# Optimization experiments

Hardware: AMD Instinct MI355X
Metric: run time of the kernel (lower is better)

Reference implementation:

```python
import jax, jax.numpy as jnp
import numpy as np

HEADS = 12
EMBED = 768
HEAD_DIM = EMBED // HEADS
SCALING = HEAD_DIM ** (-0.5)


def setup_inputs() -> dict:
    key = jax.random.key(0)
    k1, k2, k3, k4, k5 = jax.random.split(key, 5)
    B, N = 8, 1024
    x = jax.random.normal(k1, (B, N, EMBED), dtype=jnp.float32)
    W_qkv = jax.random.normal(k2, (3 * EMBED, EMBED), dtype=jnp.float32) * 0.02
    b_qkv = jax.random.normal(k3, (3 * EMBED,), dtype=jnp.float32) * 0.02
    W_proj = jax.random.normal(k4, (EMBED, EMBED), dtype=jnp.float32) * 0.02
    b_proj = jax.random.normal(k5, (EMBED,), dtype=jnp.float32) * 0.02
    return {"x": x, "W_qkv": W_qkv, "b_qkv": b_qkv, "W_proj": W_proj, "b_proj": b_proj}


def reference(x, W_qkv, b_qkv, W_proj, b_proj):
    B, N, D = x.shape
    # fused QKV projection: [B, N, 3D]
    qkv = x @ W_qkv.T + b_qkv
    # split last dim as (u=3, h, e) per einops 'b n (u h e) -> u b h n e'
    qkv = qkv.reshape(B, N, 3, HEADS, HEAD_DIM).transpose(2, 0, 3, 1, 4)
    q, k, v = qkv[0], qkv[1], qkv[2]
    # raw dot-product scores (NO pre-softmax scaling, per original)
    sim = jnp.einsum('bhqi,bhki->bhqk', q, k)
    # unusual POST-softmax scaling
    sim = jax.nn.softmax(sim, axis=-1) * SCALING
    att = jnp.einsum('bhnk,bhke->bhne', sim, v)
    att = att.transpose(0, 2, 1, 3).reshape(B, N, D)  # b h n e -> b n (h e)
    return att @ W_proj.T + b_proj
```

## Files before the change

kernel.cpp:

```cpp
#include <hip/hip_runtime.h>

typedef unsigned short u16;
typedef __attribute__((ext_vector_type(8))) short bf16x8;
typedef __attribute__((ext_vector_type(4))) float f32x4;

#define HEADS 12
#define HDIM  64
#define EMBED 768
#define TD    2304
#define SEQ   1024
#define MTOK  8192

__device__ __forceinline__ u16 f2bf(float f) {
  union { float f; unsigned u; } x; x.f = f;
  unsigned r = x.u + 0x7fffu + ((x.u >> 16) & 1u);
  return (u16)(r >> 16);
}

__global__ void cast_kernel(const float* __restrict__ src, u16* __restrict__ dst, int n4) {
  int i = blockIdx.x * blockDim.x + threadIdx.x;
  int st = gridDim.x * blockDim.x;
  for (; i < n4; i += st) {
    float4 v = reinterpret_cast<const float4*>(src)[i];
    ushort4 o;
    o.x = f2bf(v.x); o.y = f2bf(v.y); o.z = f2bf(v.z); o.w = f2bf(v.w);
    reinterpret_cast<ushort4*>(dst)[i] = o;
  }
}

__device__ __forceinline__ void gload_lds16(const u16* g, u16* l) {
  __builtin_amdgcn_global_load_lds(
      (const __attribute__((address_space(1))) unsigned*)g,
      (__attribute__((address_space(3))) unsigned*)l, 16, 0, 0);
}

template <bool OUT_BF16, bool HAS_BIAS>
__global__ __launch_bounds__(256) void gemm_bt(const u16* __restrict__ A,
                                               const u16* __restrict__ B,
                                               const float* __restrict__ bias,
                                               void* __restrict__ Cv, int K) {
  __shared__ u16 As[128 * 32];
  __shared__ u16 Bs[128 * 32];
  const int tid  = threadIdx.x;
  const int wave = tid >> 6, lane = tid & 63;
  const int wr = wave >> 1, wc = wave & 1;
  const int lr = lane & 15, lk = (lane >> 4) * 8;
  const int Ndim = gridDim.y * 128;
  const int srow = lane >> 2;
  const int scol = (lane & 3) * 8;

  const u16* Ag = A + (size_t)(blockIdx.x * 128) * K;
  const u16* Bg = B + (size_t)(blockIdx.y * 128) * K;

  f32x4 acc[4][4];
#pragma unroll
  for (int m = 0; m < 4; ++m)
#pragma unroll
    for (int n = 0; n < 4; ++n) acc[m][n] = 0.f;

  for (int kt = 0; kt < K; kt += 32) {
#pragma unroll
    for (int c = 0; c < 2; ++c) {
      int slot = wave * 2 + c;
      int row  = slot * 16 + srow;
      gload_lds16(Ag + (size_t)row * K + kt + scol, &As[slot * 512]);
      gload_lds16(Bg + (size_t)row * K + kt + scol, &Bs[slot * 512]);
    }
    __syncthreads();
    bf16x8 af[4], bfr[4];
#pragma unroll
    for (int m = 0; m < 4; ++m)
      af[m] = *reinterpret_cast<const bf16x8*>(&As[(wr * 64 + m * 16 + lr) * 32 + lk]);
#pragma unroll
    for (int n = 0; n < 4; ++n)
      bfr[n] = *reinterpret_cast<const bf16x8*>(&Bs[(wc * 64 + n * 16 + lr) * 32 + lk]);
#pragma unroll
    for (int m = 0; m < 4; ++m)
#pragma unroll
      for (int n = 0; n < 4; ++n)
        acc[m][n] = __builtin_amdgcn_mfma_f32_16x16x32_bf16(af[m], bfr[n], acc[m][n], 0, 0, 0);
    __syncthreads();
  }

  const int row0 = blockIdx.x * 128 + wr * 64 + (lane >> 4) * 4;
  const int col0 = blockIdx.y * 128 + wc * 64 + lr;
#pragma unroll
  for (int m = 0; m < 4; ++m)
#pragma unroll
    for (int n = 0; n < 4; ++n) {
      int col = col0 + n * 16;
      float bv = HAS_BIAS ? bias[col] : 0.f;
#pragma unroll
      for (int j = 0; j < 4; ++j) {
        int row = row0 + m * 16 + j;
        float v = acc[m][n][j] + bv;
        if (OUT_BF16) ((u16*)Cv)[(size_t)row * Ndim + col] = f2bf(v);
        else          ((float*)Cv)[(size_t)row * Ndim + col] = v;
      }
    }
}

__global__ __launch_bounds__(256) void vtrans_kernel(const u16* __restrict__ qkv,
                                                     u16* __restrict__ vt) {
  const int bh = blockIdx.x, kb = blockIdx.y;
  const int b = bh / HEADS, h = bh % HEADS;
  __shared__ u16 Ls[64 * 72];
  const int t = threadIdx.x;
  const int row = t >> 2, seg = t & 3;
  const u16* src = qkv + (size_t)(b * SEQ + kb * 64 + row) * TD + 2 * EMBED + h * HDIM + seg * 16;
  *reinterpret_cast<uint4*>(&Ls[row * 72 + seg * 16])     = *reinterpret_cast<const uint4*>(src);
  *reinterpret_cast<uint4*>(&Ls[row * 72 + seg * 16 + 8]) = *reinterpret_cast<const uint4*>(src + 8);
  __syncthreads();
  u16 tmp[16];
#pragma unroll
  for (int i = 0; i < 16; ++i) tmp[i] = Ls[(seg * 16 + i) * 72 + row];
  u16* dst = vt + (size_t)bh * (HDIM * SEQ) + (size_t)row * SEQ + kb * 64 + seg * 16;
  *reinterpret_cast<uint4*>(dst)     = *reinterpret_cast<const uint4*>(tmp);
  *reinterpret_cast<uint4*>(dst + 8) = *reinterpret_cast<const uint4*>(tmp + 8);
}

__global__ __launch_bounds__(256) void attn_kernel(const u16* __restrict__ qkv,
                                                   const u16* __restrict__ vt,
                                                   u16* __restrict__ ctx) {
  const int bh = blockIdx.x;
  const int b = bh / HEADS, h = bh % HEADS;
  const int qt = blockIdx.y;
  const int tid = threadIdx.x, wave = tid >> 6, lane = tid & 63;
  const int lr = lane & 15, g = lane >> 4;

  __shared__ u16 Ks[64 * 64];
  __shared__ u16 Vs[64 * 64];
  __shared__ u16 Ps[128 * 64];

  const size_t tok0 = (size_t)b * SEQ;
  const int q0 = qt * 128;
  const int mbase = wave * 32;

  bf16x8 qf[2][2];
#pragma unroll
  for (int mi = 0; mi < 2; ++mi)
#pragma unroll
    for (int dk = 0; dk < 2; ++dk)
      qf[mi][dk] = *reinterpret_cast<const bf16x8*>(
          qkv + (tok0 + q0 + mbase + mi * 16 + lr) * TD + h * HDIM + dk * 32 + g * 8);

  const int srow = lane >> 3;
  const int schunk = (lane & 7) ^ srow;

  f32x4 oacc[2][4];
#pragma unroll
  for (int mi = 0; mi < 2; ++mi)
#pragma unroll
    for (int e = 0; e < 4; ++e) oacc[mi][e] = 0.f;
  float psum[2] = {0.f, 0.f};

  for (int kb = 0; kb < 16; ++kb) {
#pragma unroll
    for (int c2 = 0; c2 < 2; ++c2) {
      int call = wave * 2 + c2;
      int row  = call * 8 + srow;
      gload_lds16(qkv + (tok0 + kb * 64 + row) * TD + EMBED + h * HDIM + schunk * 8,
                  &Ks[call * 512]);
      gload_lds16(vt + (size_t)bh * (HDIM * SEQ) + (size_t)row * SEQ + kb * 64 + schunk * 8,
                  &Vs[call * 512]);
    }
    __syncthreads();

    bf16x8 ka[4][2];
#pragma unroll
    for (int n = 0; n < 4; ++n)
#pragma unroll
      for (int dk = 0; dk < 2; ++dk) {
        int r = n * 16 + lr;
        int c = dk * 4 + g;
        ka[n][dk] = *reinterpret_cast<const bf16x8*>(&Ks[r * 64 + ((c ^ (r & 7)) << 3)]);
      }
#pragma unroll
    for (int mi = 0; mi < 2; ++mi) {
      int m = mbase + mi * 16 + lr;
      int pswz = (lr & 7) << 1;
#pragma unroll
      for (int n = 0; n < 4; ++n) {
        f32x4 s = 0.f;
        s = __builtin_amdgcn_mfma_f32_16x16x32_bf16(ka[n][0], qf[mi][0], s, 0, 0, 0);
        s = __builtin_amdgcn_mfma_f32_16x16x32_bf16(ka[n][1], qf[mi][1], s, 0, 0, 0);
        float e0 = __expf(s[0]), e1 = __expf(s[1]);
        float e2 = __expf(s[2]), e3 = __expf(s[3]);
        psum[mi] += (e0 + e1) + (e2 + e3);
        ushort4 pw;
        pw.x = f2bf(e0); pw.y = f2bf(e1); pw.z = f2bf(e2); pw.w = f2bf(e3);
        int gran = n * 4 + g;
        *reinterpret_cast<ushort4*>(&Ps[m * 64 + ((gran ^ pswz) << 2)]) = pw;
      }
    }

    bf16x8 vb2[4][2];
#pragma unroll
    for (int e = 0; e < 4; ++e)
#pragma unroll
      for (int kk = 0; kk < 2; ++kk) {
        int r = e * 16 + lr;
        int c = kk * 4 + g;
        vb2[e][kk] = *reinterpret_cast<const bf16x8*>(&Vs[r * 64 + ((c ^ (r & 7)) << 3)]);
      }
#pragma unroll
    for (int mi = 0; mi < 2; ++mi) {
      bf16x8 pa[2];
#pragma unroll
      for (int kk = 0; kk < 2; ++kk) {
        int r = mbase + mi * 16 + lr;
        int c = kk * 4 + g;
        pa[kk] = *reinterpret_cast<const bf16x8*>(&Ps[r * 64 + ((c ^ (r & 7)) << 3)]);
      }
#pragma unroll
      for (int e = 0; e < 4; ++e) {
        oacc[mi][e] = __builtin_amdgcn_mfma_f32_16x16x32_bf16(pa[0], vb2[e][0], oacc[mi][e], 0, 0, 0);
        oacc[mi][e] = __builtin_amdgcn_mfma_f32_16x16x32_bf16(pa[1], vb2[e][1], oacc[mi][e], 0, 0, 0);
      }
    }
    __syncthreads();
  }

  float scl[2][4];
#pragma unroll
  for (int mi = 0; mi < 2; ++mi) {
    float v = psum[mi];
    v += __shfl_xor(v, 16);
    v += __shfl_xor(v, 32);
    v = 0.125f / v;
#pragma unroll
    for (int j = 0; j < 4; ++j) scl[mi][j] = __shfl(v, 4 * g + j);
  }
#pragma unroll
  for (int mi = 0; mi < 2; ++mi)
#pragma unroll
    for (int e = 0; e < 4; ++e)
#pragma unroll
      for (int j = 0; j < 4; ++j) {
        float v = oacc[mi][e][j] * scl[mi][j];
        ctx[(tok0 + q0 + mbase + mi * 16 + 4 * g + j) * EMBED + h * HDIM + e * 16 + lr] = f2bf(v);
      }
}

extern "C" void kernel_launch(void* const* d_in, const int* in_sizes, int n_in,
                              void* d_out, int out_size, void* d_ws, size_t ws_size,
                              hipStream_t stream) {
  (void)in_sizes; (void)n_in; (void)out_size;
  const float* x     = (const float*)d_in[0];
  const float* Wqkv  = (const float*)d_in[1];
  const float* bqkv  = (const float*)d_in[2];
  const float* Wproj = (const float*)d_in[3];
  const float* bproj = (const float*)d_in[4];
  float* out = (float*)d_out;

  char* ws = (char*)d_ws;
  size_t off = 0;
  auto alloc = [&](size_t bytes) {
    char* p = ws + off;
    off += (bytes + 255) & ~(size_t)255;
    return p;
  };
  u16* xb     = (u16*)alloc((size_t)MTOK * EMBED * 2);
  u16* wqkvb  = (u16*)alloc((size_t)TD * EMBED * 2);
  u16* wprojb = (u16*)alloc((size_t)EMBED * EMBED * 2);
  u16* qkvb   = (u16*)alloc((size_t)MTOK * TD * 2);
  u16* ctxb   = (u16*)alloc((size_t)MTOK * EMBED * 2);
  if (off > ws_size) return;
  u16* vtb = xb;

  cast_kernel<<<dim3(1024), dim3(256), 0, stream>>>(x,     xb,     MTOK * EMBED / 4);
  cast_kernel<<<dim3(432),  dim3(256), 0, stream>>>(Wqkv,  wqkvb,  TD * EMBED / 4);
  cast_kernel<<<dim3(144),  dim3(256), 0, stream>>>(Wproj, wprojb, EMBED * EMBED / 4);

  gemm_bt<true, true><<<dim3(64, 18), dim3(256), 0, stream>>>(xb, wqkvb, bqkv, qkvb, EMBED);
  vtrans_kernel<<<dim3(96, 16), dim3(256), 0, stream>>>(qkvb, vtb);
  attn_kernel<<<dim3(96, 8), dim3(256), 0, stream>>>(qkvb, vtb, ctxb);
  gemm_bt<false, true><<<dim3(64, 6), dim3(256), 0, stream>>>(ctxb, wprojb, bproj, out, EMBED);
}
```

Measured before the change: 137.3 us.

## Double-buffer LDS tiles in GEMM and attention, widen GEMM K-tile, vectorize epilogue

The GEMM moves to a 64-wide K tile with XOR-swizzled LDS and double buffering, so the next tile's global-to-LDS load is issued before the MFMAs on the current tile. Its MFMA operands are swapped so each lane holds four consecutive output columns, which lets bias loads and output stores use float4/ushort4 vectors. The attention kernel also double-buffers its K/V tiles and wraps the MFMA blocks in s_setprio. The aim is to hide global load latency and cut scalar stores, at the cost of more LDS per block and possibly lower occupancy.

```diff
diff --git a/kernel.cpp b/kernel.cpp
--- a/kernel.cpp
+++ b/kernel.cpp
@@ -39,63 +39,90 @@
                                                const u16* __restrict__ B,
                                                const float* __restrict__ bias,
                                                void* __restrict__ Cv, int K) {
-  __shared__ u16 As[128 * 32];
-  __shared__ u16 Bs[128 * 32];
+  __shared__ u16 As[2][128 * 64];
+  __shared__ u16 Bs[2][128 * 64];
   const int tid  = threadIdx.x;
   const int wave = tid >> 6, lane = tid & 63;
   const int wr = wave >> 1, wc = wave & 1;
-  const int lr = lane & 15, lk = (lane >> 4) * 8;
+  const int lr = lane & 15, g = lane >> 4;
   const int Ndim = gridDim.y * 128;
-  const int srow = lane >> 2;
-  const int scol = (lane & 3) * 8;
 
   const u16* Ag = A + (size_t)(blockIdx.x * 128) * K;
   const u16* Bg = B + (size_t)(blockIdx.y * 128) * K;
 
+  const int srow   = lane >> 3;
+  const int schunk = (lane & 7) ^ srow;
+
   f32x4 acc[4][4];
 #pragma unroll
   for (int m = 0; m < 4; ++m)
 #pragma unroll
     for (int n = 0; n < 4; ++n) acc[m][n] = 0.f;
 
-  for (int kt = 0; kt < K; kt += 32) {
-#pragma unroll
-    for (int c = 0; c < 2; ++c) {
-      int slot = wave * 2 + c;
-      int row  = slot * 16 + srow;
-      gload_lds16(Ag + (size_t)row * K + kt + scol, &As[slot * 512]);
-      gload_lds16(Bg + (size_t)row * K + kt + scol, &Bs[slot * 512]);
-    }
-    __syncthreads();
-    bf16x8 af[4], bfr[4];
+  auto stageAB = [&](int kt, int buf) {
+#pragma unroll
+    for (int c = 0; c < 4; ++c) {
+      int slot = wave * 4 + c;
+      int row  = slot * 8 + srow;
+      gload_lds16(Ag + (size_t)row * K + kt + schunk * 8, &As[buf][slot * 512]);
+      gload_lds16(Bg + (size_t)row * K + kt + schunk * 8, &Bs[buf][slot * 512]);
+    }
+  };
+
+  const int NT = K >> 6;
+  stageAB(0, 0);
+  __syncthreads();
+  int cur = 0;
+  for (int t = 0; t < NT; ++t) {
+    if (t + 1 < NT) stageAB((t + 1) << 6, cur ^ 1);
+
+    bf16x8 af[4][2], bfr[4][2];
 #pragma unroll
     for (int m = 0; m < 4; ++m)
-      af[m] = *reinterpret_cast<const bf16x8*>(&As[(wr * 64 + m * 16 + lr) * 32 + lk]);
+#pragma unroll
+      for (int kk = 0; kk < 2; ++kk) {
+        int r = wr * 64 + m * 16 + lr;
+        af[m][kk] = *reinterpret_cast<const bf16x8*>(
+            &As[cur][r * 64 + (((kk * 4 + g) ^ (r & 7)) << 3)]);
+      }
 #pragma unroll
     for (int n = 0; n < 4; ++n)
-      bfr[n] = *reinterpret_cast<const bf16x8*>(&Bs[(wc * 64 + n * 16 + lr) * 32 + lk]);
+#pragma unroll
+      for (int kk = 0; kk < 2; ++kk) {
+        int r = wc * 64 + n * 16 + lr;
+        bfr[n][kk] = *reinterpret_cast<const bf16x8*>(
+            &Bs[cur][r * 64 + (((kk * 4 + g) ^ (r & 7)) << 3)]);
+      }
 #pragma unroll
     for (int m = 0; m < 4; ++m)
 #pragma unroll
-      for (int n = 0; n < 4; ++n)
-        acc[m][n] = __builtin_amdgcn_mfma_f32_16x16x32_bf16(af[m], bfr[n], acc[m][n], 0, 0, 0);
-    __syncthreads();
+      for (int n = 0; n < 4; ++n) {
+        acc[m][n] = __builtin_amdgcn_mfma_f32_16x16x32_bf16(bfr[n][0], af[m][0], acc[m][n], 0, 0, 0);
+        acc[m][n] = __builtin_amdgcn_mfma_f32_16x16x32_bf16(bfr[n][1], af[m][1], acc[m][n], 0, 0, 0);
+      }
+    if (t + 1 < NT) __syncthreads();
+    cur ^= 1;
   }
 
-  const int row0 = blockIdx.x * 128 + wr * 64 + (lane >> 4) * 4;
-  const int col0 = blockIdx.y * 128 + wc * 64 + lr;
+  const int row0 = blockIdx.x * 128 + wr * 64 + lr;
+  const int col0 = blockIdx.y * 128 + wc * 64 + g * 4;
 #pragma unroll
   for (int m = 0; m < 4; ++m)
 #pragma unroll
     for (int n = 0; n < 4; ++n) {
+      int row = row0 + m * 16;
       int col = col0 + n * 16;
-      float bv = HAS_BIAS ? bias[col] : 0.f;
-#pragma unroll
-      for (int j = 0; j < 4; ++j) {
-        int row = row0 + m * 16 + j;
-        float v = acc[m][n][j] + bv;
-        if (OUT_BF16) ((u16*)Cv)[(size_t)row * Ndim + col] = f2bf(v);
-        else          ((float*)Cv)[(size_t)row * Ndim + col] = v;
+      float4 bv = HAS_BIAS ? *reinterpret_cast<const float4*>(&bias[col])
+                           : make_float4(0.f, 0.f, 0.f, 0.f);
+      float v0 = acc[m][n][0] + bv.x, v1 = acc[m][n][1] + bv.y;
+      float v2 = acc[m][n][2] + bv.z, v3 = acc[m][n][3] + bv.w;
+      if (OUT_BF16) {
+        ushort4 pw;
+        pw.x = f2bf(v0); pw.y = f2bf(v1); pw.z = f2bf(v2); pw.w = f2bf(v3);
+        *reinterpret_cast<ushort4*>(&((u16*)Cv)[(size_t)row * Ndim + col]) = pw;
+      } else {
+        *reinterpret_cast<float4*>(&((float*)Cv)[(size_t)row * Ndim + col]) =
+            make_float4(v0, v1, v2, v3);
       }
     }
 }
@@ -128,8 +155,8 @@
   const int tid = threadIdx.x, wave = tid >> 6, lane = tid & 63;
   const int lr = lane & 15, g = lane >> 4;
 
-  __shared__ u16 Ks[64 * 64];
-  __shared__ u16 Vs[64 * 64];
+  __shared__ u16 Ks[2][64 * 64];
+  __shared__ u16 Vs[2][64 * 64];
   __shared__ u16 Ps[128 * 64];
 
   const size_t tok0 = (size_t)b * SEQ;
@@ -146,25 +173,32 @@
 
   const int srow = lane >> 3;
   const int schunk = (lane & 7) ^ srow;
-
-  f32x4 oacc[2][4];
-#pragma unroll
-  for (int mi = 0; mi < 2; ++mi)
-#pragma unroll
-    for (int e = 0; e < 4; ++e) oacc[mi][e] = 0.f;
-  float psum[2] = {0.f, 0.f};
-
-  for (int kb = 0; kb < 16; ++kb) {
+  const u16* vbase = vt + (size_t)bh * (HDIM * SEQ);
+
+  auto stage = [&](int kb, int buf) {
 #pragma unroll
     for (int c2 = 0; c2 < 2; ++c2) {
       int call = wave * 2 + c2;
       int row  = call * 8 + srow;
       gload_lds16(qkv + (tok0 + kb * 64 + row) * TD + EMBED + h * HDIM + schunk * 8,
-                  &Ks[call * 512]);
-      gload_lds16(vt + (size_t)bh * (HDIM * SEQ) + (size_t)row * SEQ + kb * 64 + schunk * 8,
-                  &Vs[call * 512]);
-    }
-    __syncthreads();
+                  &Ks[buf][call * 512]);
+      gload_lds16(vbase + (size_t)row * SEQ + kb * 64 + schunk * 8,
+                  &Vs[buf][call * 512]);
+    }
+  };
+
+  f32x4 oacc[2][4];
+#pragma unroll
+  for (int mi = 0; mi < 2; ++mi)
+#pragma unroll
+    for (int e = 0; e < 4; ++e) oacc[mi][e] = 0.f;
+  float psum[2] = {0.f, 0.f};
+
+  stage(0, 0);
+  __syncthreads();
+  int cur = 0;
+  for (int kb = 0; kb < 16; ++kb) {
+    if (kb < 15) stage(kb + 1, cur ^ 1);
 
     bf16x8 ka[4][2];
 #pragma unroll
@@ -173,7 +207,7 @@
       for (int dk = 0; dk < 2; ++dk) {
         int r = n * 16 + lr;
         int c = dk * 4 + g;
-        ka[n][dk] = *reinterpret_cast<const bf16x8*>(&Ks[r * 64 + ((c ^ (r & 7)) << 3)]);
+        ka[n][dk] = *reinterpret_cast<const bf16x8*>(&Ks[cur][r * 64 + ((c ^ (r & 7)) << 3)]);
       }
 #pragma unroll
     for (int mi = 0; mi < 2; ++mi) {
@@ -182,8 +216,10 @@
 #pragma unroll
       for (int n = 0; n < 4; ++n) {
         f32x4 s = 0.f;
+        __builtin_amdgcn_s_setprio(1);
         s = __builtin_amdgcn_mfma_f32_16x16x32_bf16(ka[n][0], qf[mi][0], s, 0, 0, 0);
         s = __builtin_amdgcn_mfma_f32_16x16x32_bf16(ka[n][1], qf[mi][1], s, 0, 0, 0);
+        __builtin_amdgcn_s_setprio(0);
         float e0 = __expf(s[0]), e1 = __expf(s[1]);
         float e2 = __expf(s[2]), e3 = __expf(s[3]);
         psum[mi] += (e0 + e1) + (e2 + e3);
@@ -201,7 +237,7 @@
       for (int kk = 0; kk < 2; ++kk) {
         int r = e * 16 + lr;
         int c = kk * 4 + g;
-        vb2[e][kk] = *reinterpret_cast<const bf16x8*>(&Vs[r * 64 + ((c ^ (r & 7)) << 3)]);
+        vb2[e][kk] = *reinterpret_cast<const bf16x8*>(&Vs[cur][r * 64 + ((c ^ (r & 7)) << 3)]);
       }
 #pragma unroll
     for (int mi = 0; mi < 2; ++mi) {
@@ -212,13 +248,16 @@
         int c = kk * 4 + g;
         pa[kk] = *reinterpret_cast<const bf16x8*>(&Ps[r * 64 + ((c ^ (r & 7)) << 3)]);
       }
+      __builtin_amdgcn_s_setprio(1);
 #pragma unroll
       for (int e = 0; e < 4; ++e) {
         oacc[mi][e] = __builtin_amdgcn_mfma_f32_16x16x32_bf16(pa[0], vb2[e][0], oacc[mi][e], 0, 0, 0);
         oacc[mi][e] = __builtin_amdgcn_mfma_f32_16x16x32_bf16(pa[1], vb2[e][1], oacc[mi][e], 0, 0, 0);
       }
+      __builtin_amdgcn_s_setprio(0);
     }
     __syncthreads();
+    cur ^= 1;
   }
 
   float scl[2][4];
```

After: 144.8 us. 5.5% more time.
